# Kernel tuning notes

Hardware: AMD Instinct MI355X
Metric: run time of the kernel (lower is better)

## Reference

```python
import jax, jax.numpy as jnp
import numpy as np

N, E, D, H = 50000, 400000, 128, 4
NEG_SLOPE = 0.2
LN_EPS = 1e-5


def setup_inputs() -> dict:
    key = jax.random.key(0)
    ks = jax.random.split(key, 16)
    s = 1.0 / np.sqrt(D)
    inp = {
        'x': jax.random.normal(ks[0], (N, D), jnp.float32),
        'edge_index': jax.random.randint(ks[1], (2, E), 0, N, jnp.int32),
        # GATv2Conv params: lin_l/lin_r: Linear(D, H*D), att: [H, D], bias: [D] (concat=False)
        'Wl': jax.random.normal(ks[2], (H * D, D), jnp.float32) * s,
        'bl': jnp.zeros((H * D,), jnp.float32),
        'Wr': jax.random.normal(ks[3], (H * D, D), jnp.float32) * s,
        'br': jnp.zeros((H * D,), jnp.float32),
        'att': jax.random.normal(ks[4], (H, D), jnp.float32) * s,
        'bias': jnp.zeros((D,), jnp.float32),
        # LayerNorm 1
        'g1': jnp.ones((D,), jnp.float32), 'be1': jnp.zeros((D,), jnp.float32),
        # FFN: Linear(D, 2D) -> GELU -> Linear(2D, D)
        'W1': jax.random.normal(ks[5], (2 * D, D), jnp.float32) * s,
        'b1': jnp.zeros((2 * D,), jnp.float32),
        'W2': jax.random.normal(ks[6], (D, 2 * D), jnp.float32) * (1.0 / np.sqrt(2 * D)),
        'b2': jnp.zeros((D,), jnp.float32),
        # LayerNorm 2
        'g2': jnp.ones((D,), jnp.float32), 'be2': jnp.zeros((D,), jnp.float32),
    }
    return inp


def _layernorm(x, g, b):
    mu = jnp.mean(x, -1, keepdims=True)
    var = jnp.mean(jnp.square(x - mu), -1, keepdims=True)
    return (x - mu) * jax.lax.rsqrt(var + LN_EPS) * g + b


def _gatv2(x, edge_index, Wl, bl, Wr, br, att, bias):
    # Self-loops (PyG default add_self_loops=True)
    loop = jnp.arange(N, dtype=edge_index.dtype)
    src = jnp.concatenate([edge_index[0], loop])  # [E+N]
    dst = jnp.concatenate([edge_index[1], loop])
    xl = (x @ Wl.T + bl).reshape(N, H, D)  # source transform
    xr = (x @ Wr.T + br).reshape(N, H, D)  # target transform
    m = xl[src] + xr[dst]                  # [E+N, H, D]
    e = jnp.einsum('ehd,hd->eh', jax.nn.leaky_relu(m, NEG_SLOPE), att)
    # segment softmax over destination nodes
    emax = jax.ops.segment_max(e, dst, num_segments=N)
    ee = jnp.exp(e - emax[dst])
    denom = jax.ops.segment_sum(ee, dst, num_segments=N)
    alpha = ee / (denom[dst] + 1e-16)      # [E+N, H]  (dropout=0.1 skipped: eval mode)
    out = jax.ops.segment_sum(xl[src] * alpha[:, :, None], dst, num_segments=N)
    return out.mean(axis=1) + bias         # concat=False -> head mean


def reference(x, edge_index, Wl, bl, Wr, br, att, bias, g1, be1, W1, b1, W2, b2, g2, be2):
    h = _gatv2(x, edge_index, Wl, bl, Wr, br, att, bias)
    x = _layernorm(x + h, g1, be1)
    h = jax.nn.gelu(x @ W1.T + b1, approximate=False) @ W2.T + b2
    x = _layernorm(x + h, g2, be2)
    return x
```

## Files before the change

kernel.cpp:

```cpp
#include <hip/hip_runtime.h>
#include <cstdint>
#include <cstddef>

#define N_NODES 50000
#define N_EDGES 400000
#define EN_TOT  (N_EDGES + N_NODES)
#define NC_SCAN ((N_NODES + 511) / 512)
#define NEG_SLOPE 0.2f
#define LN_EPS 1e-5f

typedef short bf16x8 __attribute__((ext_vector_type(8)));
typedef float f32x4  __attribute__((ext_vector_type(4)));

__device__ __forceinline__ ushort f2bf(float f) {
    union { float f; uint32_t u; } c; c.f = f;
    uint32_t u = c.u + 0x7FFFu + ((c.u >> 16) & 1u);
    return (ushort)(u >> 16);
}
__device__ __forceinline__ uint32_t pk2(float a, float b) {
    return (uint32_t)f2bf(a) | ((uint32_t)f2bf(b) << 16);
}
__device__ __forceinline__ float bf_lo(uint32_t u) {
    union { uint32_t u; float f; } c; c.u = u << 16; return c.f;
}
__device__ __forceinline__ float bf_hi(uint32_t u) {
    union { uint32_t u; float f; } c; c.u = u & 0xFFFF0000u; return c.f;
}

__global__ __launch_bounds__(256) void cast_weights(
    const float* __restrict__ Wl, const float* __restrict__ Wr,
    const float* __restrict__ W1, const float* __restrict__ W2,
    const float* __restrict__ att, ushort* __restrict__ wb)
{
    int i = blockIdx.x * 256 + threadIdx.x;
    const float* src; int off;
    if (i < 65536)       { src = Wl;  off = i; }
    else if (i < 131072) { src = Wr;  off = i - 65536; }
    else if (i < 163840) { src = W1;  off = i - 131072; }
    else if (i < 196608) { src = W2;  off = i - 163840; }
    else                 { src = att; off = i - 196608; }
    wb[i] = f2bf(src[off]);
}

__global__ __launch_bounds__(256) void gemm_lr(
    const float* __restrict__ x, const ushort* __restrict__ wcat,
    const float* __restrict__ bl, const float* __restrict__ br,
    ushort* __restrict__ xlb, ushort* __restrict__ xrb)
{
    __shared__ ushort As[128 * 128];
    __shared__ ushort Bs[128 * 128];
    const int tid  = threadIdx.x;
    const int rb   = blockIdx.x * 128;
    const int wave = tid >> 6, lane = tid & 63;
    const int wm   = (wave >> 1) * 64, wn = (wave & 1) * 64;
    const int lr   = lane & 15, lq = lane >> 4;

    #pragma unroll
    for (int i = 0; i < 8; ++i) {
        int chunk = tid + i * 256;
        int rr = chunk >> 4, cc = chunk & 15;
        int gr = rb + rr;
        float4 v0 = make_float4(0.f,0.f,0.f,0.f), v1 = v0;
        if (gr < N_NODES) {
            v0 = *(const float4*)(x + (size_t)gr * 128 + cc * 8);
            v1 = *(const float4*)(x + (size_t)gr * 128 + cc * 8 + 4);
        }
        uint4 h = make_uint4(pk2(v0.x,v0.y), pk2(v0.z,v0.w),
                             pk2(v1.x,v1.y), pk2(v1.z,v1.w));
        *(uint4*)(As + rr * 128 + ((cc ^ (rr & 15)) * 8)) = h;
    }

    for (int cbk = 0; cbk < 8; ++cbk) {
        __syncthreads();
        #pragma unroll
        for (int i = 0; i < 8; ++i) {
            int chunk = tid + i * 256;
            int rr = chunk >> 4, cc = chunk & 15;
            uint4 vb = *(const uint4*)(wcat + (size_t)(cbk * 128 + rr) * 128 + cc * 8);
            *(uint4*)(Bs + rr * 128 + ((cc ^ (rr & 15)) * 8)) = vb;
        }
        __syncthreads();

        f32x4 zero = {0.f,0.f,0.f,0.f};
        f32x4 acc[4][4];
        #pragma unroll
        for (int i = 0; i < 4; ++i)
            #pragma unroll
            for (int j = 0; j < 4; ++j) acc[i][j] = zero;

        #pragma unroll
        for (int q = 0; q < 4; ++q) {
            int csw = ((q * 4 + lq) ^ lr) * 8;
            bf16x8 bfr[4], af[4];
            #pragma unroll
            for (int i = 0; i < 4; ++i) {
                bfr[i] = *(const bf16x8*)(Bs + (wm + i * 16 + lr) * 128 + csw);
                af[i]  = *(const bf16x8*)(As + (wn + i * 16 + lr) * 128 + csw);
            }
            #pragma unroll
            for (int i = 0; i < 4; ++i)
                #pragma unroll
                for (int j = 0; j < 4; ++j)
                    acc[i][j] = __builtin_amdgcn_mfma_f32_16x16x32_bf16(
                        bfr[i], af[j], acc[i][j], 0, 0, 0);
        }

        const float* bias = (cbk < 4) ? bl : br;
        ushort* outp = (cbk < 4) ? xlb : xrb;
        const int cloc = (cbk & 3) * 128;
        #pragma unroll
        for (int i = 0; i < 4; ++i) {
            int wc = wm + i * 16 + lq * 4;
            float4 bv = *(const float4*)(bias + cloc + wc);
            #pragma unroll
            for (int j = 0; j < 4; ++j) {
                int node = rb + wn + j * 16 + lr;
                if (node < N_NODES) {
                    ushort4 o;
                    o.x = f2bf(acc[i][j][0] + bv.x);
                    o.y = f2bf(acc[i][j][1] + bv.y);
                    o.z = f2bf(acc[i][j][2] + bv.z);
                    o.w = f2bf(acc[i][j][3] + bv.w);
                    *(ushort4*)(outp + (size_t)node * 512 + cloc + wc) = o;
                }
            }
        }
    }
}

__global__ __launch_bounds__(256) void gemm_ffn1(
    const ushort* __restrict__ A, const ushort* __restrict__ w1b,
    const float* __restrict__ b1, ushort* __restrict__ tb)
{
    __shared__ ushort As[128 * 128];
    __shared__ ushort Bs[128 * 128];
    const int tid  = threadIdx.x;
    const int rb   = blockIdx.x * 128;
    const int wave = tid >> 6, lane = tid & 63;
    const int wm   = (wave >> 1) * 64, wn = (wave & 1) * 64;
    const int lr   = lane & 15, lq = lane >> 4;

    #pragma unroll
    for (int i = 0; i < 8; ++i) {
        int chunk = tid + i * 256;
        int rr = chunk >> 4, cc = chunk & 15;
        int gr = rb + rr;
        uint4 va = make_uint4(0u,0u,0u,0u);
        if (gr < N_NODES) va = *(const uint4*)(A + (size_t)gr * 128 + cc * 8);
        *(uint4*)(As + rr * 128 + ((cc ^ (rr & 15)) * 8)) = va;
    }

    for (int cbk = 0; cbk < 2; ++cbk) {
        __syncthreads();
        #pragma unroll
        for (int i = 0; i < 8; ++i) {
            int chunk = tid + i * 256;
            int rr = chunk >> 4, cc = chunk & 15;
            uint4 vb = *(const uint4*)(w1b + (size_t)(cbk * 128 + rr) * 128 + cc * 8);
            *(uint4*)(Bs + rr * 128 + ((cc ^ (rr & 15)) * 8)) = vb;
        }
        __syncthreads();

        f32x4 zero = {0.f,0.f,0.f,0.f};
        f32x4 acc[4][4];
        #pragma unroll
        for (int i = 0; i < 4; ++i)
            #pragma unroll
            for (int j = 0; j < 4; ++j) acc[i][j] = zero;

        #pragma unroll
        for (int q = 0; q < 4; ++q) {
            int csw = ((q * 4 + lq) ^ lr) * 8;
            bf16x8 bfr[4], af[4];
            #pragma unroll
            for (int i = 0; i < 4; ++i) {
                bfr[i] = *(const bf16x8*)(Bs + (wm + i * 16 + lr) * 128 + csw);
                af[i]  = *(const bf16x8*)(As + (wn + i * 16 + lr) * 128 + csw);
            }
            #pragma unroll
            for (int i = 0; i < 4; ++i)
                #pragma unroll
                for (int j = 0; j < 4; ++j)
                    acc[i][j] = __builtin_amdgcn_mfma_f32_16x16x32_bf16(
                        bfr[i], af[j], acc[i][j], 0, 0, 0);
        }

        const int cloc = cbk * 128;
        #pragma unroll
        for (int i = 0; i < 4; ++i) {
            int wc = wm + i * 16 + lq * 4;
            float4 bv = *(const float4*)(b1 + cloc + wc);
            #pragma unroll
            for (int j = 0; j < 4; ++j) {
                int node = rb + wn + j * 16 + lr;
                if (node < N_NODES) {
                    float v[4];
                    v[0] = acc[i][j][0] + bv.x; v[1] = acc[i][j][1] + bv.y;
                    v[2] = acc[i][j][2] + bv.z; v[3] = acc[i][j][3] + bv.w;
                    ushort4 o;
                    #pragma unroll
                    for (int r = 0; r < 4; ++r)
                        v[r] = v[r] * 0.5f * (1.0f + erff(v[r] * 0.70710678118654752f));
                    o.x = f2bf(v[0]); o.y = f2bf(v[1]);
                    o.z = f2bf(v[2]); o.w = f2bf(v[3]);
                    *(ushort4*)(tb + (size_t)node * 256 + cloc + wc) = o;
                }
            }
        }
    }
}

__global__ __launch_bounds__(256) void gemm_ffn2_ln(
    const ushort* __restrict__ tb, const ushort* __restrict__ w2b,
    const float* __restrict__ b2, const float* __restrict__ x1,
    const float* __restrict__ g2, const float* __restrict__ be2,
    float* __restrict__ out)
{
    __shared__ char smem[65536];
    ushort* As = (ushort*)smem;
    ushort* Bs = (ushort*)(smem + 32768);
    const int tid  = threadIdx.x;
    const int rb   = blockIdx.x * 128;
    const int wave = tid >> 6, lane = tid & 63;
    const int wm   = (wave >> 1) * 64, wn = (wave & 1) * 64;
    const int lr   = lane & 15, lq = lane >> 4;

    f32x4 zero = {0.f,0.f,0.f,0.f};
    f32x4 acc[4][4];
    #pragma unroll
    for (int i = 0; i < 4; ++i)
        #pragma unroll
        for (int j = 0; j < 4; ++j) acc[i][j] = zero;

    for (int k0 = 0; k0 < 256; k0 += 128) {
        __syncthreads();
        #pragma unroll
        for (int i = 0; i < 8; ++i) {
            int chunk = tid + i * 256;
            int rr = chunk >> 4, cc = chunk & 15;
            int gr = rb + rr;
            uint4 va = make_uint4(0u,0u,0u,0u);
            if (gr < N_NODES) va = *(const uint4*)(tb + (size_t)gr * 256 + k0 + cc * 8);
            *(uint4*)(As + rr * 128 + ((cc ^ (rr & 15)) * 8)) = va;
            uint4 vb = *(const uint4*)(w2b + (size_t)rr * 256 + k0 + cc * 8);
            *(uint4*)(Bs + rr * 128 + ((cc ^ (rr & 15)) * 8)) = vb;
        }
        __syncthreads();

        #pragma unroll
        for (int q = 0; q < 4; ++q) {
            int csw = ((q * 4 + lq) ^ lr) * 8;
            bf16x8 bfr[4], af[4];
            #pragma unroll
            for (int i = 0; i < 4; ++i) {
                bfr[i] = *(const bf16x8*)(Bs + (wm + i * 16 + lr) * 128 + csw);
                af[i]  = *(const bf16x8*)(As + (wn + i * 16 + lr) * 128 + csw);
            }
            #pragma unroll
            for (int i = 0; i < 4; ++i)
                #pragma unroll
                for (int j = 0; j < 4; ++j)
                    acc[i][j] = __builtin_amdgcn_mfma_f32_16x16x32_bf16(
                        bfr[i], af[j], acc[i][j], 0, 0, 0);
        }
    }

    __syncthreads();
    float* sums = (float*)smem;
    float* ssqs = (float*)(smem + 1024);

    #pragma unroll
    for (int j = 0; j < 4; ++j) {
        int node = rb + wn + j * 16 + lr;
        float s = 0.f, q2 = 0.f;
        #pragma unroll
        for (int i = 0; i < 4; ++i) {
            int wc = wm + i * 16 + lq * 4;
            float4 bv = *(const float4*)(b2 + wc);
            float4 xv = make_float4(0.f,0.f,0.f,0.f);
            if (node < N_NODES) xv = *(const float4*)(x1 + (size_t)node * 128 + wc);
            float y0 = acc[i][j][0] + bv.x + xv.x;
            float y1 = acc[i][j][1] + bv.y + xv.y;
            float y2 = acc[i][j][2] + bv.z + xv.z;
            float y3 = acc[i][j][3] + bv.w + xv.w;
            acc[i][j][0] = y0; acc[i][j][1] = y1;
            acc[i][j][2] = y2; acc[i][j][3] = y3;
            s  += y0 + y1 + y2 + y3;
            q2 += y0*y0 + y1*y1 + y2*y2 + y3*y3;
        }
        s  += __shfl_xor(s, 16, 64);  s  += __shfl_xor(s, 32, 64);
        q2 += __shfl_xor(q2, 16, 64); q2 += __shfl_xor(q2, 32, 64);
        if (lq == 0) {
            int half = wm >> 6;
            sums[half * 128 + wn + j * 16 + lr] = s;
            ssqs[half * 128 + wn + j * 16 + lr] = q2;
        }
    }
    __syncthreads();

    #pragma unroll
    for (int j = 0; j < 4; ++j) {
        int nl = wn + j * 16 + lr;
        int node = rb + nl;
        if (node >= N_NODES) continue;
        float tot = sums[nl] + sums[128 + nl];
        float tq  = ssqs[nl] + ssqs[128 + nl];
        float mu  = tot * (1.0f / 128.0f);
        float var = tq * (1.0f / 128.0f) - mu * mu;
        float rs  = rsqrtf(var + LN_EPS);
        #pragma unroll
        for (int i = 0; i < 4; ++i) {
            int wc = wm + i * 16 + lq * 4;
            float4 gv = *(const float4*)(g2 + wc);
            float4 ev = *(const float4*)(be2 + wc);
            float4 o;
            o.x = (acc[i][j][0] - mu) * rs * gv.x + ev.x;
            o.y = (acc[i][j][1] - mu) * rs * gv.y + ev.y;
            o.z = (acc[i][j][2] - mu) * rs * gv.z + ev.z;
            o.w = (acc[i][j][3] - mu) * rs * gv.w + ev.w;
            *(float4*)(out + (size_t)node * 128 + wc) = o;
        }
    }
}

__global__ __launch_bounds__(256) void count_deg(const int* __restrict__ dst,
                                                 int* __restrict__ counts)
{
    int i = blockIdx.x * 256 + threadIdx.x;
    if (i >= EN_TOT) return;
    int d = (i < N_EDGES) ? dst[i] : (i - N_EDGES);
    atomicAdd(counts + d, 1);
}

__global__ __launch_bounds__(64) void scan1(const int* __restrict__ counts,
                                            int* __restrict__ csum)
{
    int lane = threadIdx.x;
    int base = blockIdx.x * 512 + lane * 8;
    int s = 0;
    #pragma unroll
    for (int k = 0; k < 8; ++k) {
        int idx = base + k;
        if (idx < N_NODES) s += counts[idx];
    }
    #pragma unroll
    for (int m = 32; m; m >>= 1) s += __shfl_xor(s, m, 64);
    if (lane == 0) csum[blockIdx.x] = s;
}

__global__ __launch_bounds__(64) void scan2(int* __restrict__ csum,
                                            int* __restrict__ offs)
{
    int l = threadIdx.x;
    int v0 = (l < NC_SCAN) ? csum[l] : 0;
    int v1 = (l + 64 < NC_SCAN) ? csum[l + 64] : 0;
    int s0 = v0;
    #pragma unroll
    for (int d = 1; d < 64; d <<= 1) {
        int t = __shfl_up(s0, d, 64);
        if (l >= d) s0 += t;
    }
    int tot0 = __shfl(s0, 63, 64);
    int s1 = v1;
    #pragma unroll
    for (int d = 1; d < 64; d <<= 1) {
        int t = __shfl_up(s1, d, 64);
        if (l >= d) s1 += t;
    }
    int tot1 = __shfl(s1, 63, 64);
    if (l < NC_SCAN) csum[l] = s0 - v0;
    if (l + 64 < NC_SCAN) csum[l + 64] = tot0 + s1 - v1;
    if (l == 0) offs[N_NODES] = tot0 + tot1;
}

__global__ __launch_bounds__(64) void scan3(const int* __restrict__ counts,
                                            const int* __restrict__ csum,
                                            int* __restrict__ offs)
{
    int lane = threadIdx.x;
    int base = blockIdx.x * 512 + lane * 8;
    int cnt[8];
    int s = 0;
    #pragma unroll
    for (int k = 0; k < 8; ++k) {
        int idx = base + k;
        cnt[k] = (idx < N_NODES) ? counts[idx] : 0;
        s += cnt[k];
    }
    int inc = s;
    #pragma unroll
    for (int d = 1; d < 64; d <<= 1) {
        int t = __shfl_up(inc, d, 64);
        if (lane >= d) inc += t;
    }
    int run = csum[blockIdx.x] + (inc - s);
    #pragma unroll
    for (int k = 0; k < 8; ++k) {
        int idx = base + k;
        if (idx < N_NODES) { offs[idx] = run; run += cnt[k]; }
    }
}

__global__ __launch_bounds__(256) void scatter_edges(
    const int* __restrict__ src, const int* __restrict__ dst,
    const int* __restrict__ offs, int* __restrict__ cursor,
    int* __restrict__ srcList)
{
    int i = blockIdx.x * 256 + threadIdx.x;
    if (i >= EN_TOT) return;
    int s, d;
    if (i < N_EDGES) { s = src[i]; d = dst[i]; }
    else             { s = d = i - N_EDGES; }
    int pos = atomicAdd(cursor + d, 1);
    srcList[offs[d] + pos] = s;
}

__global__ __launch_bounds__(256) void gat_fused(
    const float* __restrict__ x, const ushort* __restrict__ xl,
    const ushort* __restrict__ xr, const int* __restrict__ offs,
    const int* __restrict__ srcList, const ushort* __restrict__ attb,
    const float* __restrict__ bias, const float* __restrict__ g1,
    const float* __restrict__ be1, float* __restrict__ x1,
    ushort* __restrict__ x1b)
{
    const int wave = threadIdx.x >> 6;
    const int lane = threadIdx.x & 63;
    const int v = blockIdx.x * 4 + wave;
    if (v >= N_NODES) return;

    uint4 rw = *(const uint4*)(xr + (size_t)v * 512 + lane * 8);
    uint4 aw = *(const uint4*)(attb + lane * 8);
    float r[8], at[8];
    r[0]=bf_lo(rw.x); r[1]=bf_hi(rw.x); r[2]=bf_lo(rw.y); r[3]=bf_hi(rw.y);
    r[4]=bf_lo(rw.z); r[5]=bf_hi(rw.z); r[6]=bf_lo(rw.w); r[7]=bf_hi(rw.w);
    at[0]=bf_lo(aw.x); at[1]=bf_hi(aw.x); at[2]=bf_lo(aw.y); at[3]=bf_hi(aw.y);
    at[4]=bf_lo(aw.z); at[5]=bf_hi(aw.z); at[6]=bf_lo(aw.w); at[7]=bf_hi(aw.w);

    float acc[8] = {0.f,0.f,0.f,0.f,0.f,0.f,0.f,0.f};
    float lh = 0.f;

    const int jb = offs[v], je = offs[v + 1];
    uint4 cur = *(const uint4*)(xl + (size_t)srcList[jb] * 512 + lane * 8);
    for (int j = jb; j < je; ++j) {
        int jn = (j + 1 < je) ? (j + 1) : j;
        uint4 nxt = *(const uint4*)(xl + (size_t)srcList[jn] * 512 + lane * 8);

        float b[8];
        b[0]=bf_lo(cur.x); b[1]=bf_hi(cur.x); b[2]=bf_lo(cur.y); b[3]=bf_hi(cur.y);
        b[4]=bf_lo(cur.z); b[5]=bf_hi(cur.z); b[6]=bf_lo(cur.w); b[7]=bf_hi(cur.w);
        float p = 0.f;
        #pragma unroll
        for (int k = 0; k < 8; ++k) {
            float s  = b[k] + r[k];
            float lr2 = fmaxf(s, 0.f) + NEG_SLOPE * fminf(s, 0.f);
            p = fmaf(lr2, at[k], p);
        }
        p += __shfl_xor(p, 1, 64);
        p += __shfl_xor(p, 2, 64);
        p += __shfl_xor(p, 4, 64);
        p += __shfl_xor(p, 8, 64);
        float w = __expf(p);
        lh += w;
        #pragma unroll
        for (int k = 0; k < 8; ++k) acc[k] = fmaf(w, b[k], acc[k]);
        cur = nxt;
    }

    const float inv = 1.0f / lh;
    const int d0 = (lane & 15) * 8;
    const size_t xo = (size_t)v * 128 + d0;

    float4 xv0 = *(const float4*)(x + xo);
    float4 xv1 = *(const float4*)(x + xo + 4);
    float4 bb0 = *(const float4*)(bias + d0);
    float4 bb1 = *(const float4*)(bias + d0 + 4);
    float xr8[8] = {xv0.x,xv0.y,xv0.z,xv0.w,xv1.x,xv1.y,xv1.z,xv1.w};
    float bi8[8] = {bb0.x,bb0.y,bb0.z,bb0.w,bb1.x,bb1.y,bb1.z,bb1.w};

    float y[8];
    float s = 0.f;
    #pragma unroll
    for (int k = 0; k < 8; ++k) {
        float o = acc[k] * inv;
        o += __shfl_xor(o, 16, 64);
        o += __shfl_xor(o, 32, 64);
        float yy = xr8[k] + o * 0.25f + bi8[k];
        y[k] = yy;
        s += yy;
    }
    s += __shfl_xor(s, 1, 64);
    s += __shfl_xor(s, 2, 64);
    s += __shfl_xor(s, 4, 64);
    s += __shfl_xor(s, 8, 64);
    float mu = s * (1.0f / 128.0f);
    float ss = 0.f;
    #pragma unroll
    for (int k = 0; k < 8; ++k) { float d = y[k] - mu; ss += d * d; }
    ss += __shfl_xor(ss, 1, 64);
    ss += __shfl_xor(ss, 2, 64);
    ss += __shfl_xor(ss, 4, 64);
    ss += __shfl_xor(ss, 8, 64);
    float rs = rsqrtf(ss * (1.0f / 128.0f) + LN_EPS);

    if ((lane >> 4) == 0) {
        float4 g0 = *(const float4*)(g1 + d0);
        float4 g4 = *(const float4*)(g1 + d0 + 4);
        float4 e0 = *(const float4*)(be1 + d0);
        float4 e4 = *(const float4*)(be1 + d0 + 4);
        float gg[8] = {g0.x,g0.y,g0.z,g0.w,g4.x,g4.y,g4.z,g4.w};
        float ee[8] = {e0.x,e0.y,e0.z,e0.w,e4.x,e4.y,e4.z,e4.w};
        float z[8];
        ushort4 zb0, zb1;
        #pragma unroll
        for (int k = 0; k < 8; ++k) z[k] = (y[k] - mu) * rs * gg[k] + ee[k];
        *(float4*)(x1 + xo)     = make_float4(z[0], z[1], z[2], z[3]);
        *(float4*)(x1 + xo + 4) = make_float4(z[4], z[5], z[6], z[7]);
        zb0.x=f2bf(z[0]); zb0.y=f2bf(z[1]); zb0.z=f2bf(z[2]); zb0.w=f2bf(z[3]);
        zb1.x=f2bf(z[4]); zb1.y=f2bf(z[5]); zb1.z=f2bf(z[6]); zb1.w=f2bf(z[7]);
        *(ushort4*)(x1b + xo)     = zb0;
        *(ushort4*)(x1b + xo + 4) = zb1;
    }
}

extern "C" void kernel_launch(void* const* d_in, const int* in_sizes, int n_in,
                              void* d_out, int out_size, void* d_ws, size_t ws_size,
                              hipStream_t stream)
{
    const float* x    = (const float*)d_in[0];
    const int*   ei   = (const int*)  d_in[1];
    const float* Wl   = (const float*)d_in[2];
    const float* bl   = (const float*)d_in[3];
    const float* Wr   = (const float*)d_in[4];
    const float* br   = (const float*)d_in[5];
    const float* att  = (const float*)d_in[6];
    const float* bias = (const float*)d_in[7];
    const float* g1   = (const float*)d_in[8];
    const float* be1  = (const float*)d_in[9];
    const float* W1   = (const float*)d_in[10];
    const float* b1   = (const float*)d_in[11];
    const float* W2   = (const float*)d_in[12];
    const float* b2   = (const float*)d_in[13];
    const float* g2   = (const float*)d_in[14];
    const float* be2  = (const float*)d_in[15];
    float* out = (float*)d_out;

    char* ws = (char*)d_ws;
    size_t off = 0;
    auto alloc = [&](size_t bytes) -> void* {
        void* p = ws + off;
        off = (off + bytes + 255) & ~(size_t)255;
        return p;
    };
    ushort* xlb  = (ushort*)alloc((size_t)N_NODES * 512 * 2);
    ushort* xrb  = (ushort*)alloc((size_t)N_NODES * 512 * 2);
    float*  x1   = (float*) alloc((size_t)N_NODES * 128 * 4);
    ushort* x1b  = (ushort*)alloc((size_t)N_NODES * 128 * 2);
    ushort* tb   = (ushort*)alloc((size_t)N_NODES * 256 * 2);
    ushort* wb   = (ushort*)alloc((size_t)197120 * 2);
    int*   offs    = (int*)alloc((size_t)(N_NODES + 1) * 4);
    int*   counts  = (int*)alloc((size_t)N_NODES * 4 * 2);
    int*   cursor  = counts + N_NODES;
    int*   csum    = (int*)alloc(512);
    int*   srcList = (int*)alloc((size_t)EN_TOT * 4);

    ushort* wcat = wb;
    ushort* w1b  = wb + 131072;
    ushort* w2b  = wb + 163840;
    ushort* attb = wb + 196608;

    hipMemsetAsync(counts, 0, (size_t)N_NODES * 8, stream);

    cast_weights<<<770, 256, 0, stream>>>(Wl, Wr, W1, W2, att, wb);

    gemm_lr<<<391, 256, 0, stream>>>(x, wcat, bl, br, xlb, xrb);

    count_deg<<<(EN_TOT + 255) / 256, 256, 0, stream>>>(ei + N_EDGES, counts);
    scan1<<<NC_SCAN, 64, 0, stream>>>(counts, csum);
    scan2<<<1, 64, 0, stream>>>(csum, offs);
    scan3<<<NC_SCAN, 64, 0, stream>>>(counts, csum, offs);
    scatter_edges<<<(EN_TOT + 255) / 256, 256, 0, stream>>>(ei, ei + N_EDGES,
                                                           offs, cursor, srcList);

    gat_fused<<<12500, 256, 0, stream>>>(x, xlb, xrb, offs, srcList, attb,
                                         bias, g1, be1, x1, x1b);

    gemm_ffn1<<<391, 256, 0, stream>>>(x1b, w1b, b1, tb);
    gemm_ffn2_ln<<<391, 256, 0, stream>>>(tb, w2b, b2, x1, g2, be2, out);
}
```

Measured before the change: 323.7 us.

## Fuse FFN GEMMs, merge scans, split LR GEMM grid, unroll GAT edges

Merges the two FFN GEMMs into one kernel that keeps the GELU intermediate in shared memory, so the N×256 intermediate no longer round-trips through global memory. Replaces the three-kernel scan with a single-block scan. Splits gemm_lr across a second grid dimension for more parallelism, and unrolls the GAT edge loop by two. It also drops the fp32 x1 buffer and uses the bf16 copy as the residual input to the second LayerNorm. That trims traffic but lowers residual precision, and the kernel needs 96 KB of shared memory, which may reduce occupancy.

```diff
diff --git a/kernel.cpp b/kernel.cpp
--- a/kernel.cpp
+++ b/kernel.cpp
@@ -5,7 +5,6 @@
 #define N_NODES 50000
 #define N_EDGES 400000
 #define EN_TOT  (N_EDGES + N_NODES)
-#define NC_SCAN ((N_NODES + 511) / 512)
 #define NEG_SLOPE 0.2f
 #define LN_EPS 1e-5f
 
@@ -25,6 +24,9 @@
 }
 __device__ __forceinline__ float bf_hi(uint32_t u) {
     union { uint32_t u; float f; } c; c.u = u & 0xFFFF0000u; return c.f;
+}
+__device__ __forceinline__ float bfu(const ushort* p) {
+    union { uint32_t u; float f; } c; c.u = ((uint32_t)*p) << 16; return c.f;
 }
 
 __global__ __launch_bounds__(256) void cast_weights(
@@ -55,6 +57,10 @@
     const int wm   = (wave >> 1) * 64, wn = (wave & 1) * 64;
     const int lr   = lane & 15, lq = lane >> 4;
 
+    const float* bias = (blockIdx.y == 0) ? bl : br;
+    ushort* outp      = (blockIdx.y == 0) ? xlb : xrb;
+    const int cbk0    = blockIdx.y * 4;
+
     #pragma unroll
     for (int i = 0; i < 8; ++i) {
         int chunk = tid + i * 256;
@@ -70,7 +76,8 @@
         *(uint4*)(As + rr * 128 + ((cc ^ (rr & 15)) * 8)) = h;
     }
 
-    for (int cbk = 0; cbk < 8; ++cbk) {
+    for (int t = 0; t < 4; ++t) {
+        int cbk = cbk0 + t;
         __syncthreads();
         #pragma unroll
         for (int i = 0; i < 8; ++i) {
@@ -105,8 +112,6 @@
                         bfr[i], af[j], acc[i][j], 0, 0, 0);
         }
 
-        const float* bias = (cbk < 4) ? bl : br;
-        ushort* outp = (cbk < 4) ? xlb : xrb;
         const int cloc = (cbk & 3) * 128;
         #pragma unroll
         for (int i = 0; i < 4; ++i) {
@@ -128,12 +133,212 @@
     }
 }
 
-__global__ __launch_bounds__(256) void gemm_ffn1(
-    const ushort* __restrict__ A, const ushort* __restrict__ w1b,
-    const float* __restrict__ b1, ushort* __restrict__ tb)
+__global__ __launch_bounds__(256) void count_deg(const int* __restrict__ dst,
+                                                 int* __restrict__ counts)
+{
+    int i = blockIdx.x * 256 + threadIdx.x;
+    if (i >= EN_TOT) return;
+    int d = (i < N_EDGES) ? dst[i] : (i - N_EDGES);
+    atomicAdd(counts + d, 1);
+}
+
+__global__ __launch_bounds__(1024) void scan_all(const int* __restrict__ counts,
+                                                 int* __restrict__ offs)
+{
+    __shared__ int wsum[16];
+    __shared__ int wpre[16];
+    const int t = threadIdx.x;
+    const int lane = t & 63, w = t >> 6;
+    const int C = 49;
+    const int base = t * C;
+
+    int s = 0;
+    for (int k = 0; k < C; ++k) {
+        int idx = base + k;
+        if (idx < N_NODES) s += counts[idx];
+    }
+    int inc = s;
+    #pragma unroll
+    for (int d = 1; d < 64; d <<= 1) {
+        int v = __shfl_up(inc, d, 64);
+        if (lane >= d) inc += v;
+    }
+    if (lane == 63) wsum[w] = inc;
+    __syncthreads();
+    if (t < 16) {
+        int v = wsum[t];
+        int p = v;
+        #pragma unroll
+        for (int d = 1; d < 16; d <<= 1) {
+            int q = __shfl_up(p, d, 64);
+            if (t >= d) p += q;
+        }
+        wpre[t] = p - v;
+    }
+    __syncthreads();
+    int run = wpre[w] + (inc - s);
+    for (int k = 0; k < C; ++k) {
+        int idx = base + k;
+        if (idx < N_NODES) { offs[idx] = run; run += counts[idx]; }
+    }
+    if (t == 1023) offs[N_NODES] = wpre[15] + inc;
+}
+
+__global__ __launch_bounds__(256) void scatter_edges(
+    const int* __restrict__ src, const int* __restrict__ dst,
+    const int* __restrict__ offs, int* __restrict__ cursor,
+    int* __restrict__ srcList)
+{
+    int i = blockIdx.x * 256 + threadIdx.x;
+    if (i >= EN_TOT) return;
+    int s, d;
+    if (i < N_EDGES) { s = src[i]; d = dst[i]; }
+    else             { s = d = i - N_EDGES; }
+    int pos = atomicAdd(cursor + d, 1);
+    srcList[offs[d] + pos] = s;
+}
+
+__global__ __launch_bounds__(256) void gat_fused(
+    const float* __restrict__ x, const ushort* __restrict__ xl,
+    const ushort* __restrict__ xr, const int* __restrict__ offs,
+    const int* __restrict__ srcList, const ushort* __restrict__ attb,
+    const float* __restrict__ bias, const float* __restrict__ g1,
+    const float* __restrict__ be1, ushort* __restrict__ x1b)
+{
+    const int wave = threadIdx.x >> 6;
+    const int lane = threadIdx.x & 63;
+    const int v = blockIdx.x * 4 + wave;
+    if (v >= N_NODES) return;
+
+    uint4 rw = *(const uint4*)(xr + (size_t)v * 512 + lane * 8);
+    uint4 aw = *(const uint4*)(attb + lane * 8);
+    float r[8], at[8];
+    r[0]=bf_lo(rw.x); r[1]=bf_hi(rw.x); r[2]=bf_lo(rw.y); r[3]=bf_hi(rw.y);
+    r[4]=bf_lo(rw.z); r[5]=bf_hi(rw.z); r[6]=bf_lo(rw.w); r[7]=bf_hi(rw.w);
+    at[0]=bf_lo(aw.x); at[1]=bf_hi(aw.x); at[2]=bf_lo(aw.y); at[3]=bf_hi(aw.y);
+    at[4]=bf_lo(aw.z); at[5]=bf_hi(aw.z); at[6]=bf_lo(aw.w); at[7]=bf_hi(aw.w);
+
+    float acc[8] = {0.f,0.f,0.f,0.f,0.f,0.f,0.f,0.f};
+    float lh = 0.f;
+
+    const int jb = offs[v], je = offs[v + 1];
+    int j = jb;
+    while (j + 1 < je) {
+        int u0 = srcList[j], u1 = srcList[j + 1];
+        uint4 c0 = *(const uint4*)(xl + (size_t)u0 * 512 + lane * 8);
+        uint4 c1 = *(const uint4*)(xl + (size_t)u1 * 512 + lane * 8);
+        float b0[8], b1[8];
+        b0[0]=bf_lo(c0.x); b0[1]=bf_hi(c0.x); b0[2]=bf_lo(c0.y); b0[3]=bf_hi(c0.y);
+        b0[4]=bf_lo(c0.z); b0[5]=bf_hi(c0.z); b0[6]=bf_lo(c0.w); b0[7]=bf_hi(c0.w);
+        b1[0]=bf_lo(c1.x); b1[1]=bf_hi(c1.x); b1[2]=bf_lo(c1.y); b1[3]=bf_hi(c1.y);
+        b1[4]=bf_lo(c1.z); b1[5]=bf_hi(c1.z); b1[6]=bf_lo(c1.w); b1[7]=bf_hi(c1.w);
+        float p0 = 0.f, p1 = 0.f;
+        #pragma unroll
+        for (int k = 0; k < 8; ++k) {
+            float s0 = b0[k] + r[k];
+            float s1 = b1[k] + r[k];
+            float l0 = fmaxf(s0, 0.f) + NEG_SLOPE * fminf(s0, 0.f);
+            float l1 = fmaxf(s1, 0.f) + NEG_SLOPE * fminf(s1, 0.f);
+            p0 = fmaf(l0, at[k], p0);
+            p1 = fmaf(l1, at[k], p1);
+        }
+        p0 += __shfl_xor(p0, 1, 64);  p1 += __shfl_xor(p1, 1, 64);
+        p0 += __shfl_xor(p0, 2, 64);  p1 += __shfl_xor(p1, 2, 64);
+        p0 += __shfl_xor(p0, 4, 64);  p1 += __shfl_xor(p1, 4, 64);
+        p0 += __shfl_xor(p0, 8, 64);  p1 += __shfl_xor(p1, 8, 64);
+        float w0 = __expf(p0), w1 = __expf(p1);
+        lh += w0 + w1;
+        #pragma unroll
+        for (int k = 0; k < 8; ++k)
+            acc[k] = fmaf(w0, b0[k], fmaf(w1, b1[k], acc[k]));
+        j += 2;
+    }
+    if (j < je) {
+        int u0 = srcList[j];
+        uint4 c0 = *(const uint4*)(xl + (size_t)u0 * 512 + lane * 8);
+        float b0[8];
+        b0[0]=bf_lo(c0.x); b0[1]=bf_hi(c0.x); b0[2]=bf_lo(c0.y); b0[3]=bf_hi(c0.y);
+        b0[4]=bf_lo(c0.z); b0[5]=bf_hi(c0.z); b0[6]=bf_lo(c0.w); b0[7]=bf_hi(c0.w);
+        float p0 = 0.f;
+        #pragma unroll
+        for (int k = 0; k < 8; ++k) {
+            float s0 = b0[k] + r[k];
+            float l0 = fmaxf(s0, 0.f) + NEG_SLOPE * fminf(s0, 0.f);
+            p0 = fmaf(l0, at[k], p0);
+        }
+        p0 += __shfl_xor(p0, 1, 64);
+        p0 += __shfl_xor(p0, 2, 64);
+        p0 += __shfl_xor(p0, 4, 64);
+        p0 += __shfl_xor(p0, 8, 64);
+        float w0 = __expf(p0);
+        lh += w0;
+        #pragma unroll
+        for (int k = 0; k < 8; ++k) acc[k] = fmaf(w0, b0[k], acc[k]);
+    }
+
+    const float inv = 1.0f / lh;
+    const int d0 = (lane & 15) * 8;
+    const size_t xo = (size_t)v * 128 + d0;
+
+    float4 xv0 = *(const float4*)(x + xo);
+    float4 xv1 = *(const float4*)(x + xo + 4);
+    float4 bb0 = *(const float4*)(bias + d0);
+    float4 bb1 = *(const float4*)(bias + d0 + 4);
+    float xr8[8] = {xv0.x,xv0.y,xv0.z,xv0.w,xv1.x,xv1.y,xv1.z,xv1.w};
+    float bi8[8] = {bb0.x,bb0.y,bb0.z,bb0.w,bb1.x,bb1.y,bb1.z,bb1.w};
+
+    float y[8];
+    float s = 0.f;
+    #pragma unroll
+    for (int k = 0; k < 8; ++k) {
+        float o = acc[k] * inv;
+        o += __shfl_xor(o, 16, 64);
+        o += __shfl_xor(o, 32, 64);
+        float yy = xr8[k] + o * 0.25f + bi8[k];
+        y[k] = yy;
+        s += yy;
+    }
+    s += __shfl_xor(s, 1, 64);
+    s += __shfl_xor(s, 2, 64);
+    s += __shfl_xor(s, 4, 64);
+    s += __shfl_xor(s, 8, 64);
+    float mu = s * (1.0f / 128.0f);
+    float ss = 0.f;
+    #pragma unroll
+    for (int k = 0; k < 8; ++k) { float d = y[k] - mu; ss += d * d; }
+    ss += __shfl_xor(ss, 1, 64);
+    ss += __shfl_xor(ss, 2, 64);
+    ss += __shfl_xor(ss, 4, 64);
+    ss += __shfl_xor(ss, 8, 64);
+    float rs = rsqrtf(ss * (1.0f / 128.0f) + LN_EPS);
+
+    if ((lane >> 4) == 0) {
+        float4 g0 = *(const float4*)(g1 + d0);
+        float4 g4 = *(const float4*)(g1 + d0 + 4);
+        float4 e0 = *(const float4*)(be1 + d0);
+        float4 e4 = *(const float4*)(be1 + d0 + 4);
+        float gg[8] = {g0.x,g0.y,g0.z,g0.w,g4.x,g4.y,g4.z,g4.w};
+        float ee[8] = {e0.x,e0.y,e0.z,e0.w,e4.x,e4.y,e4.z,e4.w};
+        float z[8];
+        #pragma unroll
+        for (int k = 0; k < 8; ++k) z[k] = (y[k] - mu) * rs * gg[k] + ee[k];
+        ushort4 zb0, zb1;
+        zb0.x=f2bf(z[0]); zb0.y=f2bf(z[1]); zb0.z=f2bf(z[2]); zb0.w=f2bf(z[3]);
+        zb1.x=f2bf(z[4]); zb1.y=f2bf(z[5]); zb1.z=f2bf(z[6]); zb1.w=f2bf(z[7]);
+        *(ushort4*)(x1b + xo)     = zb0;
+        *(ushort4*)(x1b + xo + 4) = zb1;
+    }
+}
+
+__global__ __launch_bounds__(256) void ffn_fused(
+    const ushort* __restrict__ x1b, const ushort* __restrict__ w1b,
+    const float* __restrict__ b1, const ushort* __restrict__ w2b,
+    const float* __restrict__ b2, const float* __restrict__ g2,
+    const float* __restrict__ be2, float* __restrict__ out)
 {
     __shared__ ushort As[128 * 128];
     __shared__ ushort Bs[128 * 128];
+    __shared__ ushort Ts[128 * 128];
     const int tid  = threadIdx.x;
     const int rb   = blockIdx.x * 128;
     const int wave = tid >> 6, lane = tid & 63;
@@ -146,27 +351,33 @@
         int rr = chunk >> 4, cc = chunk & 15;
         int gr = rb + rr;
         uint4 va = make_uint4(0u,0u,0u,0u);
-        if (gr < N_NODES) va = *(const uint4*)(A + (size_t)gr * 128 + cc * 8);
+        if (gr < N_NODES) va = *(const uint4*)(x1b + (size_t)gr * 128 + cc * 8);
         *(uint4*)(As + rr * 128 + ((cc ^ (rr & 15)) * 8)) = va;
     }
 
-    for (int cbk = 0; cbk < 2; ++cbk) {
+    f32x4 zero = {0.f,0.f,0.f,0.f};
+    f32x4 acc2[4][4];
+    #pragma unroll
+    for (int i = 0; i < 4; ++i)
+        #pragma unroll
+        for (int j = 0; j < 4; ++j) acc2[i][j] = zero;
+
+    for (int half = 0; half < 2; ++half) {
         __syncthreads();
         #pragma unroll
         for (int i = 0; i < 8; ++i) {
             int chunk = tid + i * 256;
             int rr = chunk >> 4, cc = chunk & 15;
-            uint4 vb = *(const uint4*)(w1b + (size_t)(cbk * 128 + rr) * 128 + cc * 8);
+            uint4 vb = *(const uint4*)(w1b + (size_t)(half * 128 + rr) * 128 + cc * 8);
             *(uint4*)(Bs + rr * 128 + ((cc ^ (rr & 15)) * 8)) = vb;
         }
         __syncthreads();
 
-        f32x4 zero = {0.f,0.f,0.f,0.f};
-        f32x4 acc[4][4];
+        f32x4 acc1[4][4];
         #pragma unroll
         for (int i = 0; i < 4; ++i)
             #pragma unroll
-            for (int j = 0; j < 4; ++j) acc[i][j] = zero;
+            for (int j = 0; j < 4; ++j) acc1[i][j] = zero;
 
         #pragma unroll
         for (int q = 0; q < 4; ++q) {
@@ -181,68 +392,37 @@
             for (int i = 0; i < 4; ++i)
                 #pragma unroll
                 for (int j = 0; j < 4; ++j)
-                    acc[i][j] = __builtin_amdgcn_mfma_f32_16x16x32_bf16(
-                        bfr[i], af[j], acc[i][j], 0, 0, 0);
-        }
-
-        const int cloc = cbk * 128;
+                    acc1[i][j] = __builtin_amdgcn_mfma_f32_16x16x32_bf16(
+                        bfr[i], af[j], acc1[i][j], 0, 0, 0);
+        }
+
         #pragma unroll
         for (int i = 0; i < 4; ++i) {
             int wc = wm + i * 16 + lq * 4;
-            float4 bv = *(const float4*)(b1 + cloc + wc);
+            float4 bv = *(const float4*)(b1 + half * 128 + wc);
             #pragma unroll
             for (int j = 0; j < 4; ++j) {
-                int node = rb + wn + j * 16 + lr;
-                if (node < N_NODES) {
-                    float v[4];
-                    v[0] = acc[i][j][0] + bv.x; v[1] = acc[i][j][1] + bv.y;
-                    v[2] = acc[i][j][2] + bv.z; v[3] = acc[i][j][3] + bv.w;
-                    ushort4 o;
-                    #pragma unroll
-                    for (int r = 0; r < 4; ++r)
-                        v[r] = v[r] * 0.5f * (1.0f + erff(v[r] * 0.70710678118654752f));
-                    o.x = f2bf(v[0]); o.y = f2bf(v[1]);
-                    o.z = f2bf(v[2]); o.w = f2bf(v[3]);
-                    *(ushort4*)(tb + (size_t)node * 256 + cloc + wc) = o;
-                }
+                int nl = wn + j * 16 + lr;
+                float v0 = acc1[i][j][0] + bv.x;
+                float v1 = acc1[i][j][1] + bv.y;
+                float v2 = acc1[i][j][2] + bv.z;
+                float v3 = acc1[i][j][3] + bv.w;
+                v0 = v0 * 0.5f * (1.0f + erff(v0 * 0.70710678118654752f));
+                v1 = v1 * 0.5f * (1.0f + erff(v1 * 0.70710678118654752f));
+                v2 = v2 * 0.5f * (1.0f + erff(v2 * 0.70710678118654752f));
+                v3 = v3 * 0.5f * (1.0f + erff(v3 * 0.70710678118654752f));
+                ushort4 o;
+                o.x = f2bf(v0); o.y = f2bf(v1); o.z = f2bf(v2); o.w = f2bf(v3);
+                int sw = (((wc >> 3) ^ (nl & 15)) * 8) + (wc & 7);
+                *(ushort4*)(Ts + nl * 128 + sw) = o;
             }
         }
-    }
-}
-
-__global__ __launch_bounds__(256) void gemm_ffn2_ln(
-    const ushort* __restrict__ tb, const ushort* __restrict__ w2b,
-    const float* __restrict__ b2, const float* __restrict__ x1,
-    const float* __restrict__ g2, const float* __restrict__ be2,
-    float* __restrict__ out)
-{
-    __shared__ char smem[65536];
-    ushort* As = (ushort*)smem;
-    ushort* Bs = (ushort*)(smem + 32768);
-    const int tid  = threadIdx.x;
-    const int rb   = blockIdx.x * 128;
-    const int wave = tid >> 6, lane = tid & 63;
-    const int wm   = (wave >> 1) * 64, wn = (wave & 1) * 64;
-    const int lr   = lane & 15, lq = lane >> 4;
-
-    f32x4 zero = {0.f,0.f,0.f,0.f};
-    f32x4 acc[4][4];
-    #pragma unroll
-    for (int i = 0; i < 4; ++i)
-        #pragma unroll
-        for (int j = 0; j < 4; ++j) acc[i][j] = zero;
-
-    for (int k0 = 0; k0 < 256; k0 += 128) {
         __syncthreads();
         #pragma unroll
         for (int i = 0; i < 8; ++i) {
             int chunk = tid + i * 256;
             int rr = chunk >> 4, cc = chunk & 15;
-            int gr = rb + rr;
-            uint4 va = make_uint4(0u,0u,0u,0u);
-            if (gr < N_NODES) va = *(const uint4*)(tb + (size_t)gr * 256 + k0 + cc * 8);
-            *(uint4*)(As + rr * 128 + ((cc ^ (rr & 15)) * 8)) = va;
-            uint4 vb = *(const uint4*)(w2b + (size_t)rr * 256 + k0 + cc * 8);
+            uint4 vb = *(const uint4*)(w2b + (size_t)rr * 256 + half * 128 + cc * 8);
             *(uint4*)(Bs + rr * 128 + ((cc ^ (rr & 15)) * 8)) = vb;
         }
         __syncthreads();
@@ -254,20 +434,20 @@
             #pragma unroll
             for (int i = 0; i < 4; ++i) {
                 bfr[i] = *(const bf16x8*)(Bs + (wm + i * 16 + lr) * 128 + csw);
-                af[i]  = *(const bf16x8*)(As + (wn + i * 16 + lr) * 128 + csw);
+                af[i]  = *(const bf16x8*)(Ts + (wn + i * 16 + lr) * 128 + csw);
             }
             #pragma unroll
             for (int i = 0; i < 4; ++i)
                 #pragma unroll
                 for (int j = 0; j < 4; ++j)
-                    acc[i][j] = __builtin_amdgcn_mfma_f32_16x16x32_bf16(
-                        bfr[i], af[j], acc[i][j], 0, 0, 0);
+                    acc2[i][j] = __builtin_amdgcn_mfma_f32_16x16x32_bf16(
+                        bfr[i], af[j], acc2[i][j], 0, 0, 0);
         }
     }
 
     __syncthreads();
-    float* sums = (float*)smem;
-    float* ssqs = (float*)(smem + 1024);
+    float* sums = (float*)As;
+    float* ssqs = (float*)(As + 2048);
 
     #pragma unroll
     for (int j = 0; j < 4; ++j) {
@@ -277,14 +457,17 @@
         for (int i = 0; i < 4; ++i) {
             int wc = wm + i * 16 + lq * 4;
             float4 bv = *(const float4*)(b2 + wc);
-            float4 xv = make_float4(0.f,0.f,0.f,0.f);
-            if (node < N_NODES) xv = *(const float4*)(x1 + (size_t)node * 128 + wc);
-            float y0 = acc[i][j][0] + bv.x + xv.x;
-            float y1 = acc[i][j][1] + bv.y + xv.y;
-            float y2 = acc[i][j][2] + bv.z + xv.z;
-            float y3 = acc[i][j][3] + bv.w + xv.w;
-            acc[i][j][0] = y0; acc[i][j][1] = y1;
-            acc[i][j][2] = y2; acc[i][j][3] = y3;
+            float x0 = 0.f, x1r = 0.f, x2 = 0.f, x3 = 0.f;
+            if (node < N_NODES) {
+                ushort4 xv = *(const ushort4*)(x1b + (size_t)node * 128 + wc);
+                x0 = bfu(&xv.x); x1r = bfu(&xv.y); x2 = bfu(&xv.z); x3 = bfu(&xv.w);
+            }
+            float y0 = acc2[i][j][0] + bv.x + x0;
+            float y1 = acc2[i][j][1] + bv.y + x1r;
+            float y2 = acc2[i][j][2] + bv.z + x2;
+            float y3 = acc2[i][j][3] + bv.w + x3;
+            acc2[i][j][0] = y0; acc2[i][j][1] = y1;
+            acc2[i][j][2] = y2; acc2[i][j][3] = y3;
             s  += y0 + y1 + y2 + y3;
             q2 += y0*y0 + y1*y1 + y2*y2 + y3*y3;
         }
@@ -314,211 +497,12 @@
             float4 gv = *(const float4*)(g2 + wc);
             float4 ev = *(const float4*)(be2 + wc);
             float4 o;
-            o.x = (acc[i][j][0] - mu) * rs * gv.x + ev.x;
-            o.y = (acc[i][j][1] - mu) * rs * gv.y + ev.y;
-            o.z = (acc[i][j][2] - mu) * rs * gv.z + ev.z;
-            o.w = (acc[i][j][3] - mu) * rs * gv.w + ev.w;
+            o.x = (acc2[i][j][0] - mu) * rs * gv.x + ev.x;
+            o.y = (acc2[i][j][1] - mu) * rs * gv.y + ev.y;
+            o.z = (acc2[i][j][2] - mu) * rs * gv.z + ev.z;
+            o.w = (acc2[i][j][3] - mu) * rs * gv.w + ev.w;
             *(float4*)(out + (size_t)node * 128 + wc) = o;
         }
-    }
-}
-
-__global__ __launch_bounds__(256) void count_deg(const int* __restrict__ dst,
-                                                 int* __restrict__ counts)
-{
-    int i = blockIdx.x * 256 + threadIdx.x;
-    if (i >= EN_TOT) return;
-    int d = (i < N_EDGES) ? dst[i] : (i - N_EDGES);
-    atomicAdd(counts + d, 1);
-}
-
-__global__ __launch_bounds__(64) void scan1(const int* __restrict__ counts,
-                                            int* __restrict__ csum)
-{
-    int lane = threadIdx.x;
-    int base = blockIdx.x * 512 + lane * 8;
-    int s = 0;
-    #pragma unroll
-    for (int k = 0; k < 8; ++k) {
-        int idx = base + k;
-        if (idx < N_NODES) s += counts[idx];
-    }
-    #pragma unroll
-    for (int m = 32; m; m >>= 1) s += __shfl_xor(s, m, 64);
-    if (lane == 0) csum[blockIdx.x] = s;
-}
-
-__global__ __launch_bounds__(64) void scan2(int* __restrict__ csum,
-                                            int* __restrict__ offs)
-{
-    int l = threadIdx.x;
-    int v0 = (l < NC_SCAN) ? csum[l] : 0;
-    int v1 = (l + 64 < NC_SCAN) ? csum[l + 64] : 0;
-    int s0 = v0;
-    #pragma unroll
-    for (int d = 1; d < 64; d <<= 1) {
-        int t = __shfl_up(s0, d, 64);
-        if (l >= d) s0 += t;
-    }
-    int tot0 = __shfl(s0, 63, 64);
-    int s1 = v1;
-    #pragma unroll
-    for (int d = 1; d < 64; d <<= 1) {
-        int t = __shfl_up(s1, d, 64);
-        if (l >= d) s1 += t;
-    }
-    int tot1 = __shfl(s1, 63, 64);
-    if (l < NC_SCAN) csum[l] = s0 - v0;
-    if (l + 64 < NC_SCAN) csum[l + 64] = tot0 + s1 - v1;
-    if (l == 0) offs[N_NODES] = tot0 + tot1;
-}
-
-__global__ __launch_bounds__(64) void scan3(const int* __restrict__ counts,
-                                            const int* __restrict__ csum,
-                                            int* __restrict__ offs)
-{
-    int lane = threadIdx.x;
-    int base = blockIdx.x * 512 + lane * 8;
-    int cnt[8];
-    int s = 0;
-    #pragma unroll
-    for (int k = 0; k < 8; ++k) {
-        int idx = base + k;
-        cnt[k] = (idx < N_NODES) ? counts[idx] : 0;
-        s += cnt[k];
-    }
-    int inc = s;
-    #pragma unroll
-    for (int d = 1; d < 64; d <<= 1) {
-        int t = __shfl_up(inc, d, 64);
-        if (lane >= d) inc += t;
-    }
-    int run = csum[blockIdx.x] + (inc - s);
-    #pragma unroll
-    for (int k = 0; k < 8; ++k) {
-        int idx = base + k;
-        if (idx < N_NODES) { offs[idx] = run; run += cnt[k]; }
-    }
-}
-
-__global__ __launch_bounds__(256) void scatter_edges(
-    const int* __restrict__ src, const int* __restrict__ dst,
-    const int* __restrict__ offs, int* __restrict__ cursor,
-    int* __restrict__ srcList)
-{
-    int i = blockIdx.x * 256 + threadIdx.x;
-    if (i >= EN_TOT) return;
-    int s, d;
-    if (i < N_EDGES) { s = src[i]; d = dst[i]; }
-    else             { s = d = i - N_EDGES; }
-    int pos = atomicAdd(cursor + d, 1);
-    srcList[offs[d] + pos] = s;
-}
-
-__global__ __launch_bounds__(256) void gat_fused(
-    const float* __restrict__ x, const ushort* __restrict__ xl,
-    const ushort* __restrict__ xr, const int* __restrict__ offs,
-    const int* __restrict__ srcList, const ushort* __restrict__ attb,
-    const float* __restrict__ bias, const float* __restrict__ g1,
-    const float* __restrict__ be1, float* __restrict__ x1,
-    ushort* __restrict__ x1b)
-{
-    const int wave = threadIdx.x >> 6;
-    const int lane = threadIdx.x & 63;
-    const int v = blockIdx.x * 4 + wave;
-    if (v >= N_NODES) return;
-
-    uint4 rw = *(const uint4*)(xr + (size_t)v * 512 + lane * 8);
-    uint4 aw = *(const uint4*)(attb + lane * 8);
-    float r[8], at[8];
-    r[0]=bf_lo(rw.x); r[1]=bf_hi(rw.x); r[2]=bf_lo(rw.y); r[3]=bf_hi(rw.y);
-    r[4]=bf_lo(rw.z); r[5]=bf_hi(rw.z); r[6]=bf_lo(rw.w); r[7]=bf_hi(rw.w);
-    at[0]=bf_lo(aw.x); at[1]=bf_hi(aw.x); at[2]=bf_lo(aw.y); at[3]=bf_hi(aw.y);
-    at[4]=bf_lo(aw.z); at[5]=bf_hi(aw.z); at[6]=bf_lo(aw.w); at[7]=bf_hi(aw.w);
-
-    float acc[8] = {0.f,0.f,0.f,0.f,0.f,0.f,0.f,0.f};
-    float lh = 0.f;
-
-    const int jb = offs[v], je = offs[v + 1];
-    uint4 cur = *(const uint4*)(xl + (size_t)srcList[jb] * 512 + lane * 8);
-    for (int j = jb; j < je; ++j) {
-        int jn = (j + 1 < je) ? (j + 1) : j;
-        uint4 nxt = *(const uint4*)(xl + (size_t)srcList[jn] * 512 + lane * 8);
-
-        float b[8];
-        b[0]=bf_lo(cur.x); b[1]=bf_hi(cur.x); b[2]=bf_lo(cur.y); b[3]=bf_hi(cur.y);
-        b[4]=bf_lo(cur.z); b[5]=bf_hi(cur.z); b[6]=bf_lo(cur.w); b[7]=bf_hi(cur.w);
-        float p = 0.f;
-        #pragma unroll
-        for (int k = 0; k < 8; ++k) {
-            float s  = b[k] + r[k];
-            float lr2 = fmaxf(s, 0.f) + NEG_SLOPE * fminf(s, 0.f);
-            p = fmaf(lr2, at[k], p);
-        }
-        p += __shfl_xor(p, 1, 64);
-        p += __shfl_xor(p, 2, 64);
-        p += __shfl_xor(p, 4, 64);
-        p += __shfl_xor(p, 8, 64);
-        float w = __expf(p);
-        lh += w;
-        #pragma unroll
-        for (int k = 0; k < 8; ++k) acc[k] = fmaf(w, b[k], acc[k]);
-        cur = nxt;
-    }
-
-    const float inv = 1.0f / lh;
-    const int d0 = (lane & 15) * 8;
-    const size_t xo = (size_t)v * 128 + d0;
-
-    float4 xv0 = *(const float4*)(x + xo);
-    float4 xv1 = *(const float4*)(x + xo + 4);
-    float4 bb0 = *(const float4*)(bias + d0);
-    float4 bb1 = *(const float4*)(bias + d0 + 4);
-    float xr8[8] = {xv0.x,xv0.y,xv0.z,xv0.w,xv1.x,xv1.y,xv1.z,xv1.w};
-    float bi8[8] = {bb0.x,bb0.y,bb0.z,bb0.w,bb1.x,bb1.y,bb1.z,bb1.w};
-
-    float y[8];
-    float s = 0.f;
-    #pragma unroll
-    for (int k = 0; k < 8; ++k) {
-        float o = acc[k] * inv;
-        o += __shfl_xor(o, 16, 64);
-        o += __shfl_xor(o, 32, 64);
-        float yy = xr8[k] + o * 0.25f + bi8[k];
-        y[k] = yy;
-        s += yy;
-    }
-    s += __shfl_xor(s, 1, 64);
-    s += __shfl_xor(s, 2, 64);
-    s += __shfl_xor(s, 4, 64);
-    s += __shfl_xor(s, 8, 64);
-    float mu = s * (1.0f / 128.0f);
-    float ss = 0.f;
-    #pragma unroll
-    for (int k = 0; k < 8; ++k) { float d = y[k] - mu; ss += d * d; }
-    ss += __shfl_xor(ss, 1, 64);
-    ss += __shfl_xor(ss, 2, 64);
-    ss += __shfl_xor(ss, 4, 64);
-    ss += __shfl_xor(ss, 8, 64);
-    float rs = rsqrtf(ss * (1.0f / 128.0f) + LN_EPS);
-
-    if ((lane >> 4) == 0) {
-        float4 g0 = *(const float4*)(g1 + d0);
-        float4 g4 = *(const float4*)(g1 + d0 + 4);
-        float4 e0 = *(const float4*)(be1 + d0);
-        float4 e4 = *(const float4*)(be1 + d0 + 4);
-        float gg[8] = {g0.x,g0.y,g0.z,g0.w,g4.x,g4.y,g4.z,g4.w};
-        float ee[8] = {e0.x,e0.y,e0.z,e0.w,e4.x,e4.y,e4.z,e4.w};
-        float z[8];
-        ushort4 zb0, zb1;
-        #pragma unroll
-        for (int k = 0; k < 8; ++k) z[k] = (y[k] - mu) * rs * gg[k] + ee[k];
-        *(float4*)(x1 + xo)     = make_float4(z[0], z[1], z[2], z[3]);
-        *(float4*)(x1 + xo + 4) = make_float4(z[4], z[5], z[6], z[7]);
-        zb0.x=f2bf(z[0]); zb0.y=f2bf(z[1]); zb0.z=f2bf(z[2]); zb0.w=f2bf(z[3]);
-        zb1.x=f2bf(z[4]); zb1.y=f2bf(z[5]); zb1.z=f2bf(z[6]); zb1.w=f2bf(z[7]);
-        *(ushort4*)(x1b + xo)     = zb0;
-        *(ushort4*)(x1b + xo + 4) = zb1;
     }
 }
 
@@ -553,14 +537,11 @@
     };
     ushort* xlb  = (ushort*)alloc((size_t)N_NODES * 512 * 2);
     ushort* xrb  = (ushort*)alloc((size_t)N_NODES * 512 * 2);
-    float*  x1   = (float*) alloc((size_t)N_NODES * 128 * 4);
     ushort* x1b  = (ushort*)alloc((size_t)N_NODES * 128 * 2);
-    ushort* tb   = (ushort*)alloc((size_t)N_NODES * 256 * 2);
     ushort* wb   = (ushort*)alloc((size_t)197120 * 2);
     int*   offs    = (int*)alloc((size_t)(N_NODES + 1) * 4);
     int*   counts  = (int*)alloc((size_t)N_NODES * 4 * 2);
     int*   cursor  = counts + N_NODES;
-    int*   csum    = (int*)alloc(512);
     int*   srcList = (int*)alloc((size_t)EN_TOT * 4);
 
     ushort* wcat = wb;
@@ -572,18 +553,15 @@
 
     cast_weights<<<770, 256, 0, stream>>>(Wl, Wr, W1, W2, att, wb);
 
-    gemm_lr<<<391, 256, 0, stream>>>(x, wcat, bl, br, xlb, xrb);
+    gemm_lr<<<dim3(391, 2), 256, 0, stream>>>(x, wcat, bl, br, xlb, xrb);
 
     count_deg<<<(EN_TOT + 255) / 256, 256, 0, stream>>>(ei + N_EDGES, counts);
-    scan1<<<NC_SCAN, 64, 0, stream>>>(counts, csum);
-    scan2<<<1, 64, 0, stream>>>(csum, offs);
-    scan3<<<NC_SCAN, 64, 0, stream>>>(counts, csum, offs);
+    scan_all<<<1, 1024, 0, stream>>>(counts, offs);
     scatter_edges<<<(EN_TOT + 255) / 256, 256, 0, stream>>>(ei, ei + N_EDGES,
                                                            offs, cursor, srcList);
 
     gat_fused<<<12500, 256, 0, stream>>>(x, xlb, xrb, offs, srcList, attb,
-                                         bias, g1, be1, x1, x1b);
-
-    gemm_ffn1<<<391, 256, 0, stream>>>(x1b, w1b, b1, tb);
-    gemm_ffn2_ln<<<391, 256, 0, stream>>>(tb, w2b, b2, x1, g2, be2, out);
-}
+                                         bias, g1, be1, x1b);
+
+    ffn_fused<<<391, 256, 0, stream>>>(x1b, w1b, b1, w2b, b2, g2, be2, out);
+}
```

Result: slower. 416.9 us (+28.8%).
